# Optimization experiments

Measured on AMD Instinct MI355X. Metric: run time of the kernel, lower is better.

## Reference

```python
import jax, jax.numpy as jnp
import numpy as np
from jax import lax

VTH = 0.5
GRAD_WIN = 0.5
CDECAY = 0.5
VDECAY = 0.75

@jax.custom_vjp
def pseudo_spike(v):
    # PseudoSpikeRect: heaviside fwd, rectangular surrogate grad bwd
    return (v > VTH).astype(v.dtype)

def _ps_fwd(v):
    return pseudo_spike(v), v

def _ps_bwd(v, g):
    return (g * (jnp.abs(v - VTH) < GRAD_WIN).astype(g.dtype),)

pseudo_spike.defvjp(_ps_fwd, _ps_bwd)

def conv2d(x, w, b):
    y = lax.conv_general_dilated(x, w, (1, 1), 'VALID',
                                 dimension_numbers=('NCHW', 'OIHW', 'NCHW'))
    return y + b[None, :, None, None]

def lif(psp, state):
    # CUBA-LIF: current decay + integrate, voltage decay with spike reset, threshold
    cur, volt, spk = state
    cur = CDECAY * cur + psp
    volt = VDECAY * volt * (1.0 - spk) + cur
    spk = pseudo_spike(volt)
    return spk, (cur, volt, spk)

def setup_inputs() -> dict:
    key = jax.random.key(0)
    ks = jax.random.split(key, 16)
    B, T = 64, 200
    c1, c2, c3 = 64, 128, 256
    s = lambda k, shape, scale: jax.random.normal(k, shape, jnp.float32) * scale
    return {
        'input_data': jax.random.normal(ks[0], (B, 1, 10, 10, T), jnp.float32),
        'conv1_w': s(ks[1], (c1, 1, 3, 3), 0.3), 'conv1_b': s(ks[2], (c1,), 0.1),
        'conv2_w': s(ks[3], (c2, c1, 3, 3), 0.05), 'conv2_b': s(ks[4], (c2,), 0.1),
        'conv3_w': s(ks[5], (c3, c2, 3, 3), 0.03), 'conv3_b': s(ks[6], (c3,), 0.1),
        'tc_w': s(ks[7], (3, c3, c3), 0.06), 'tc_b': s(ks[8], (3, c3), 0.1),
        'rec_w': s(ks[9], (c3, c3), 0.06), 'rec_b': s(ks[10], (c3,), 0.1),
        'fc1_w': s(ks[11], (128, c3), 0.06), 'fc1_b': s(ks[12], (128,), 0.1),
        'fc2_w': s(ks[13], (2, 128), 0.09),
        'ts_weights': jnp.ones((T, 1), jnp.float32) / T,
    }

def reference(input_data, conv1_w, conv1_b, conv2_w, conv2_b, conv3_w, conv3_b,
              tc_w, tc_b, rec_w, rec_b, fc1_w, fc1_b, fc2_w, ts_weights):
    B = input_data.shape[0]
    c1, c2, c3 = conv1_w.shape[0], conv2_w.shape[0], conv3_w.shape[0]
    f1 = fc1_w.shape[0]

    def zs(shape):
        z = jnp.zeros(shape, input_data.dtype)
        return (z, z, z)

    carry0 = (zs((B, c1, 8, 8)), zs((B, c2, 6, 6)), zs((B, c3, 1, 1)),
              zs((B, c3)), zs((B, c3)), zs((B, f1)),
              jnp.zeros((3, B, c3), input_data.dtype),  # temporal buffer, idx0 = newest
              jnp.int32(0))
    xs = jnp.moveaxis(input_data, -1, 0)  # [T, B, 1, 10, 10]

    def step_fn(carry, xw):
        c1_st, c2_st, c3_st, tc_st, r_st, f_st, buf, step = carry
        x, w = xw
        s1, c1_st = lif(conv2d(x, conv1_w, conv1_b), c1_st)       # [B,c1,8,8]
        s2, c2_st = lif(conv2d(s1, conv2_w, conv2_b), c2_st)      # [B,c2,6,6]
        p = s2.reshape(B, c2, 3, 2, 3, 2).mean(axis=(3, 5))       # AvgPool2d(2) -> [B,c2,3,3]
        s3, c3_st = lif(conv2d(p, conv3_w, conv3_b), c3_st)       # [B,c3,1,1]
        flat = s3.reshape(B, -1)                                   # [B,c3]
        buf = jnp.concatenate([flat[None], buf[:2]], axis=0)
        # temporal conv: tap i applies to spike at time t-i, only if it exists
        psp = jnp.zeros_like(flat)
        for i in range(3):
            tap = buf[i] @ tc_w[i].T + tc_b[i]
            psp = psp + jnp.where(step >= i, 1.0, 0.0).astype(tap.dtype) * tap
        s_tc, tc_st = lif(psp, tc_st)
        # recurrent cell: identity feedforward + linear on previous spike
        psp_r = s_tc + r_st[2] @ rec_w.T + rec_b
        s_r, r_st = lif(psp_r, r_st)
        s_f, f_st = lif(s_r @ fc1_w.T + fc1_b, f_st)
        out = (s_f @ fc2_w.T) * w  # w = ts_weights[step], shape [1]
        return (c1_st, c2_st, c3_st, tc_st, r_st, f_st, buf, step + 1), out

    _, outs = lax.scan(step_fn, carry0, (xs, ts_weights))
    return outs.sum(axis=0)  # [B, 2]
```

## Files before the change

kernel.cpp:

```cpp
#include <hip/hip_runtime.h>


#define B_   64
#define T_   200
#define TCB_ 50

__device__ __forceinline__ void lif32(float psp, float& cur, float& volt, float& spk) {
#pragma clang fp contract(off)
    cur  = __fadd_rn(__fmul_rn(0.5f, cur), psp);
    volt = __fadd_rn(__fmul_rn(__fmul_rn(0.75f, volt), __fsub_rn(1.0f, spk)), cur);
    spk  = (volt > 0.5f) ? 1.0f : 0.0f;
}

__global__ void k_setup(const float* __restrict__ w2, const float* __restrict__ w3,
                        const float* __restrict__ tcw, const float* __restrict__ recw,
                        const float* __restrict__ fw,
                        float* __restrict__ w2T, float* __restrict__ w3T,
                        float* __restrict__ tcT, float* __restrict__ recT,
                        float* __restrict__ fc1T) {
    int idx = blockIdx.x * 256 + threadIdx.x;
    if (idx < 73728) { int o = idx & 127, k = idx >> 7; w2T[idx] = w2[o * 576 + k]; return; }
    idx -= 73728;
    if (idx < 294912) { int o = idx & 255, k = idx >> 8; w3T[idx] = w3[o * 1152 + k]; return; }
    idx -= 294912;
    if (idx < 196608) { int tap = idx >> 16, r = idx & 65535; int o = r & 255, k = r >> 8;
                        tcT[idx] = tcw[tap * 65536 + o * 256 + k]; return; }
    idx -= 196608;
    if (idx < 65536) { int o = idx & 255, k = idx >> 8; recT[idx] = recw[o * 256 + k]; return; }
    idx -= 65536;
    if (idx < 32768) { int o = idx & 127, k = idx >> 7; fc1T[idx] = fw[o * 256 + k]; return; }
}

__global__ __launch_bounds__(256) void k_conv1(const float* __restrict__ x,
                                               const float* __restrict__ w1,
                                               const float* __restrict__ b1,
                                               unsigned char* __restrict__ s1c,
                                               float* __restrict__ st1,
                                               int t0, int TC, int first) {
    int idx = blockIdx.x * 256 + threadIdx.x;
    int xx = idx & 7, yy = (idx >> 3) & 7, o = (idx >> 6) & 63, b = idx >> 12;
    float w[9];
#pragma unroll
    for (int i = 0; i < 9; i++) w[i] = w1[o * 9 + i];
    float bias = b1[o];
    const float* xb = x + (size_t)b * 20000;
    unsigned char* sb = s1c + (size_t)b * TC * 4096 + (o << 6) + (yy << 3) + xx;
    float cur, volt, spk;
    if (first) { cur = 0.f; volt = 0.f; spk = 0.f; }
    else { cur = st1[idx]; volt = st1[262144 + idx]; spk = st1[524288 + idx]; }
    for (int tl = 0; tl < TC; tl += 4) {
        int t = t0 + tl;
        float a0 = 0.f, a1 = 0.f, a2 = 0.f, a3 = 0.f;
#pragma unroll
        for (int i = 0; i < 3; i++) {
#pragma unroll
            for (int j = 0; j < 3; j++) {
                float4 v = *(const float4*)&xb[((yy + i) * 10 + xx + j) * T_ + t];
                float wv = w[i * 3 + j];
                a0 = fmaf(wv, v.x, a0); a1 = fmaf(wv, v.y, a1);
                a2 = fmaf(wv, v.z, a2); a3 = fmaf(wv, v.w, a3);
            }
        }
        float accs[4] = {a0, a1, a2, a3};
#pragma unroll
        for (int q = 0; q < 4; q++) {
            float psp = __fadd_rn(accs[q], bias);
            lif32(psp, cur, volt, spk);
            sb[(size_t)(tl + q) * 4096] = (unsigned char)spk;
        }
    }
    st1[idx] = cur; st1[262144 + idx] = volt; st1[524288 + idx] = spk;
}

__global__ __launch_bounds__(192) void k_conv2(const unsigned char* __restrict__ s1c,
                                               const float* __restrict__ w2T,
                                               const float* __restrict__ b2,
                                               float* __restrict__ psp2c) {
    __shared__ float a_s[4096];
    int blk = blockIdx.x;
    int tid = threadIdx.x;
    const unsigned int* src4 = (const unsigned int*)(s1c + (size_t)blk * 4096);
    for (int i = tid; i < 1024; i += 192) {
        unsigned int u = src4[i];
        a_s[4 * i + 0] = (float)(u & 0xff);
        a_s[4 * i + 1] = (float)((u >> 8) & 0xff);
        a_s[4 * i + 2] = (float)((u >> 16) & 0xff);
        a_s[4 * i + 3] = (float)(u >> 24);
    }
    __syncthreads();
    int quad = tid / 6;
    int y = tid - quad * 6;
    int ob = quad << 2;
    float acc[4][6];
#pragma unroll
    for (int oo = 0; oo < 4; oo++)
#pragma unroll
        for (int xq = 0; xq < 6; xq++) acc[oo][xq] = 0.f;
    for (int c = 0; c < 64; c++) {
#pragma unroll
        for (int i = 0; i < 3; i++) {
            const float* ar = &a_s[c * 64 + (y + i) * 8];
            float4 f0 = *(const float4*)(ar);
            float4 f1 = *(const float4*)(ar + 4);
            float a[8] = {f0.x, f0.y, f0.z, f0.w, f1.x, f1.y, f1.z, f1.w};
            const float* wr = w2T + (size_t)((c * 3 + i) * 3) * 128 + ob;
#pragma unroll
            for (int j = 0; j < 3; j++) {
                float4 wv = *(const float4*)(wr + j * 128);
                float w4[4] = {wv.x, wv.y, wv.z, wv.w};
#pragma unroll
                for (int oo = 0; oo < 4; oo++)
#pragma unroll
                    for (int xq = 0; xq < 6; xq++)
                        acc[oo][xq] = fmaf(w4[oo], a[xq + j], acc[oo][xq]);
            }
        }
    }
    size_t obase = (size_t)blk * 4608 + (size_t)ob * 36 + y * 6;
#pragma unroll
    for (int oo = 0; oo < 4; oo++) {
        float bv = b2[ob + oo];
        float* dst = psp2c + obase + oo * 36;
#pragma unroll
        for (int xq = 0; xq < 6; xq++)
            dst[xq] = __fadd_rn(acc[oo][xq], bv);
    }
}

__global__ __launch_bounds__(256) void k_lif2pool(const float* __restrict__ psp2c,
                                                  float* __restrict__ pc,
                                                  float* __restrict__ st2,
                                                  int TC, int first) {
    int idx = blockIdx.x * 256 + threadIdx.x;
    int px = idx % 3; int r = idx / 3; int py = r % 3; r /= 3;
    int o = r & 127, b = r >> 7;
    const float* pb = psp2c + (size_t)b * TC * 4608 + o * 36;
    float* pd = pc + (size_t)b * TC * 1152 + o * 9 + py * 3 + px;
    int off0 = (2 * py) * 6 + 2 * px, off1 = off0 + 6;
    float c0, c1, c2, c3, v0, v1, v2, v3, s0, s1, s2, s3;
    if (first) {
        c0 = c1 = c2 = c3 = v0 = v1 = v2 = v3 = s0 = s1 = s2 = s3 = 0.f;
    } else {
        c0 = st2[idx];              c1 = st2[73728 + idx];
        c2 = st2[147456 + idx];     c3 = st2[221184 + idx];
        v0 = st2[294912 + idx];     v1 = st2[368640 + idx];
        v2 = st2[442368 + idx];     v3 = st2[516096 + idx];
        s0 = st2[589824 + idx];     s1 = st2[663552 + idx];
        s2 = st2[737280 + idx];     s3 = st2[811008 + idx];
    }
    for (int tl = 0; tl < TC; tl++) {
        const float* pt = pb + (size_t)tl * 4608;
        float2 ra = *(const float2*)(pt + off0);
        float2 rb = *(const float2*)(pt + off1);
        lif32(ra.x, c0, v0, s0);
        lif32(ra.y, c1, v1, s1);
        lif32(rb.x, c2, v2, s2);
        lif32(rb.y, c3, v3, s3);
        pd[(size_t)tl * 1152] = __fmul_rn(0.25f, __fadd_rn(__fadd_rn(__fadd_rn(s0, s1), s2), s3));
    }
    st2[idx] = c0;           st2[73728 + idx] = c1;
    st2[147456 + idx] = c2;  st2[221184 + idx] = c3;
    st2[294912 + idx] = v0;  st2[368640 + idx] = v1;
    st2[442368 + idx] = v2;  st2[516096 + idx] = v3;
    st2[589824 + idx] = s0;  st2[663552 + idx] = s1;
    st2[737280 + idx] = s2;  st2[811008 + idx] = s3;
}

__global__ __launch_bounds__(256) void k_conv3(const float* __restrict__ pc,
                                               const float* __restrict__ w3T,
                                               const float* __restrict__ b3,
                                               float* __restrict__ psp3c) {
    __shared__ float a_s[16 * 288];
    int row0 = blockIdx.x * 16;
    int tid = threadIdx.x;
    int oq = tid & 63, mg = tid >> 6;
    float acc[4][4];
#pragma unroll
    for (int oo = 0; oo < 4; oo++)
#pragma unroll
        for (int mi = 0; mi < 4; mi++) acc[oo][mi] = 0.f;
    for (int kc = 0; kc < 1152; kc += 288) {
        __syncthreads();
        for (int idx = tid; idx < 16 * 288; idx += 256) {
            int m = idx / 288, k = idx - m * 288;
            a_s[idx] = pc[(size_t)(row0 + m) * 1152 + kc + k];
        }
        __syncthreads();
        for (int k = 0; k < 288; k++) {
            float4 wv = *(const float4*)&w3T[(size_t)(kc + k) * 256 + (oq << 2)];
            float w4[4] = {wv.x, wv.y, wv.z, wv.w};
            float am[4];
#pragma unroll
            for (int mi = 0; mi < 4; mi++) am[mi] = a_s[(mg * 4 + mi) * 288 + k];
#pragma unroll
            for (int oo = 0; oo < 4; oo++)
#pragma unroll
                for (int mi = 0; mi < 4; mi++)
                    acc[oo][mi] = fmaf(w4[oo], am[mi], acc[oo][mi]);
        }
    }
#pragma unroll
    for (int mi = 0; mi < 4; mi++) {
        float* dst = psp3c + (size_t)(row0 + mg * 4 + mi) * 256 + (oq << 2);
#pragma unroll
        for (int oo = 0; oo < 4; oo++)
            dst[oo] = __fadd_rn(acc[oo][mi], b3[(oq << 2) + oo]);
    }
}

__global__ __launch_bounds__(256) void k_scan3(const float* __restrict__ psp3c,
                                               unsigned char* __restrict__ s3u8,
                                               float* __restrict__ st3,
                                               int t0, int TC, int first) {
    int idx = blockIdx.x * 256 + threadIdx.x;
    int b = idx >> 8, n = idx & 255;
    float cur, volt, spk;
    if (first) { cur = 0.f; volt = 0.f; spk = 0.f; }
    else { cur = st3[idx]; volt = st3[16384 + idx]; spk = st3[32768 + idx]; }
    for (int tl = 0; tl < TC; tl++) {
        lif32(psp3c[(size_t)(b * TC + tl) * 256 + n], cur, volt, spk);
        s3u8[((size_t)b * T_ + t0 + tl) * 256 + n] = (unsigned char)spk;
    }
    st3[idx] = cur; st3[16384 + idx] = volt; st3[32768 + idx] = spk;
}

__global__ __launch_bounds__(256) void k_tc(const unsigned char* __restrict__ s3u8,
                                            const float* __restrict__ tcT,
                                            const float* __restrict__ tc_b,
                                            float* __restrict__ ptcc, int t0) {
    __shared__ float a_s[16 * 256];
    int crow0 = blockIdx.x * 16;
    int tid = threadIdx.x;
    int oq = tid & 63, mg = tid >> 6;
    float psum[4][4];
#pragma unroll
    for (int oo = 0; oo < 4; oo++)
#pragma unroll
        for (int mi = 0; mi < 4; mi++) psum[oo][mi] = 0.f;
    for (int tap = 0; tap < 3; tap++) {
        __syncthreads();
        for (int idx = tid; idx < 16 * 256; idx += 256) {
            int m = idx >> 8, k = idx & 255;
            int crow = crow0 + m;
            int b = crow / TCB_, tl = crow - b * TCB_;
            int t = t0 + tl;
            float v = 0.f;
            if (t >= tap) v = (float)s3u8[((size_t)b * T_ + t - tap) * 256 + k];
            a_s[idx] = v;
        }
        __syncthreads();
        float acc[4][4];
#pragma unroll
        for (int oo = 0; oo < 4; oo++)
#pragma unroll
            for (int mi = 0; mi < 4; mi++) acc[oo][mi] = 0.f;
        const float* wbase = tcT + (size_t)tap * 65536 + (oq << 2);
        for (int k = 0; k < 256; k++) {
            float4 wv = *(const float4*)(wbase + (size_t)k * 256);
            float w4[4] = {wv.x, wv.y, wv.z, wv.w};
            float am[4];
#pragma unroll
            for (int mi = 0; mi < 4; mi++) am[mi] = a_s[(mg * 4 + mi) * 256 + k];
#pragma unroll
            for (int oo = 0; oo < 4; oo++)
#pragma unroll
                for (int mi = 0; mi < 4; mi++)
                    acc[oo][mi] = fmaf(w4[oo], am[mi], acc[oo][mi]);
        }
#pragma unroll
        for (int mi = 0; mi < 4; mi++) {
            int crow = crow0 + mg * 4 + mi;
            int b = crow / TCB_, tl = crow - b * TCB_;
            int t = t0 + tl;
            float g = (t >= tap) ? 1.0f : 0.0f;
#pragma unroll
            for (int oo = 0; oo < 4; oo++) {
                int oc = (oq << 2) + oo;
                float tap_f = __fadd_rn(acc[oo][mi], tc_b[tap * 256 + oc]);
                psum[oo][mi] = __fadd_rn(psum[oo][mi], __fmul_rn(g, tap_f));
            }
        }
    }
#pragma unroll
    for (int mi = 0; mi < 4; mi++) {
        int crow = crow0 + mg * 4 + mi;
        float* dst = ptcc + (size_t)crow * 256 + (oq << 2);
#pragma unroll
        for (int oo = 0; oo < 4; oo++) dst[oo] = psum[oo][mi];
    }
}

__global__ __launch_bounds__(256) void k_scan_tc(const float* __restrict__ ptcc,
                                                 unsigned char* __restrict__ s_tc8,
                                                 float* __restrict__ st_tc,
                                                 int t0, int first) {
    int idx = blockIdx.x * 256 + threadIdx.x;
    int b = idx >> 8, n = idx & 255;
    float cur, volt, spk;
    if (first) { cur = 0.f; volt = 0.f; spk = 0.f; }
    else { cur = st_tc[idx]; volt = st_tc[16384 + idx]; spk = st_tc[32768 + idx]; }
    for (int tl = 0; tl < TCB_; tl++) {
        lif32(ptcc[(size_t)(b * TCB_ + tl) * 256 + n], cur, volt, spk);
        s_tc8[((size_t)b * T_ + t0 + tl) * 256 + n] = (unsigned char)spk;
    }
    st_tc[idx] = cur; st_tc[16384 + idx] = volt; st_tc[32768 + idx] = spk;
}

__global__ __launch_bounds__(256, 1) void k_rec(const unsigned char* __restrict__ s_tc8,
                                                const float* __restrict__ recT,
                                                const float* __restrict__ rec_b,
                                                unsigned char* __restrict__ s_r8) {
    __shared__ __align__(16) float spk_s[2][256];
    int b = blockIdx.x, o = threadIdx.x;
    float w[256];
#pragma unroll
    for (int k = 0; k < 256; k++) w[k] = recT[(size_t)k * 256 + o];
    spk_s[0][o] = 0.f;
    float cur = 0.f, volt = 0.f, spk = 0.f;
    float rb = rec_b[o];
    const unsigned char* stp = s_tc8 + (size_t)b * T_ * 256 + o;
    unsigned char* srp = s_r8 + (size_t)b * T_ * 256 + o;
    __syncthreads();
    int p = 0;
    for (int t = 0; t < T_; t++) {
        float stc = (float)stp[(size_t)t * 256];
        const float* sp = spk_s[p];
        float acc = 0.f;
#pragma unroll
        for (int k = 0; k < 256; k += 4) {
            float4 sv = *(const float4*)&sp[k];
            acc = fmaf(sv.x, w[k + 0], acc);
            acc = fmaf(sv.y, w[k + 1], acc);
            acc = fmaf(sv.z, w[k + 2], acc);
            acc = fmaf(sv.w, w[k + 3], acc);
        }
        float psp = __fadd_rn(__fadd_rn(stc, acc), rb);
        lif32(psp, cur, volt, spk);
        srp[(size_t)t * 256] = (unsigned char)spk;
        spk_s[p ^ 1][o] = spk;
        __syncthreads();
        p ^= 1;
    }
}

__global__ __launch_bounds__(256) void k_fc1(const unsigned char* __restrict__ s_r8,
                                             const float* __restrict__ fc1T,
                                             const float* __restrict__ fc1_b,
                                             float* __restrict__ pfc, int t0) {
    __shared__ float a_s[16 * 256];
    int crow0 = blockIdx.x * 16;
    int tid = threadIdx.x;
    int oq = tid & 31, mg = tid >> 5;
    float acc[4][2];
#pragma unroll
    for (int oo = 0; oo < 4; oo++) { acc[oo][0] = 0.f; acc[oo][1] = 0.f; }
    for (int idx = tid; idx < 16 * 256; idx += 256) {
        int m = idx >> 8, k = idx & 255;
        int crow = crow0 + m;
        int b = crow / TCB_, tl = crow - b * TCB_;
        a_s[idx] = (float)s_r8[((size_t)b * T_ + t0 + tl) * 256 + k];
    }
    __syncthreads();
    for (int k = 0; k < 256; k++) {
        float4 wv = *(const float4*)&fc1T[(size_t)k * 128 + (oq << 2)];
        float w4[4] = {wv.x, wv.y, wv.z, wv.w};
        float a0 = a_s[(mg * 2 + 0) * 256 + k];
        float a1 = a_s[(mg * 2 + 1) * 256 + k];
#pragma unroll
        for (int oo = 0; oo < 4; oo++) {
            acc[oo][0] = fmaf(w4[oo], a0, acc[oo][0]);
            acc[oo][1] = fmaf(w4[oo], a1, acc[oo][1]);
        }
    }
#pragma unroll
    for (int mi = 0; mi < 2; mi++) {
        float* dst = pfc + (size_t)(crow0 + mg * 2 + mi) * 128 + (oq << 2);
#pragma unroll
        for (int oo = 0; oo < 4; oo++)
            dst[oo] = __fadd_rn(acc[oo][mi], fc1_b[(oq << 2) + oo]);
    }
}

__global__ __launch_bounds__(256) void k_scan_f(const float* __restrict__ pfc,
                                                unsigned char* __restrict__ s_f8,
                                                float* __restrict__ st_f,
                                                int t0, int first) {
    int idx = blockIdx.x * 256 + threadIdx.x;
    int b = idx >> 7, n = idx & 127;
    float cur, volt, spk;
    if (first) { cur = 0.f; volt = 0.f; spk = 0.f; }
    else { cur = st_f[idx]; volt = st_f[8192 + idx]; spk = st_f[16384 + idx]; }
    for (int tl = 0; tl < TCB_; tl++) {
        lif32(pfc[(size_t)(b * TCB_ + tl) * 128 + n], cur, volt, spk);
        s_f8[((size_t)b * T_ + t0 + tl) * 128 + n] = (unsigned char)spk;
    }
    st_f[idx] = cur; st_f[8192 + idx] = volt; st_f[16384 + idx] = spk;
}

__global__ __launch_bounds__(128) void k_final(const unsigned char* __restrict__ s_f8,
                                               const float* __restrict__ ts,
                                               const float* __restrict__ fc2,
                                               float* __restrict__ out) {
    __shared__ double q_s[128];
    int b = blockIdx.x, k = threadIdx.x;
    double q = 0.0;
    const unsigned char* sf = s_f8 + (size_t)b * T_ * 128 + k;
    for (int t = 0; t < T_; t++) q = fma((double)ts[t], (double)sf[(size_t)t * 128], q);
    q_s[k] = q;
    __syncthreads();
    if (k < 2) {
        double o = 0.0;
        for (int kk = 0; kk < 128; kk++) o = fma((double)fc2[k * 128 + kk], q_s[kk], o);
        out[b * 2 + k] = (float)o;
    }
}

extern "C" void kernel_launch(void* const* d_in, const int* in_sizes, int n_in,
                              void* d_out, int out_size, void* d_ws, size_t ws_size,
                              hipStream_t stream) {
    const float* x       = (const float*)d_in[0];
    const float* conv1_w = (const float*)d_in[1];
    const float* conv1_b = (const float*)d_in[2];
    const float* conv2_w = (const float*)d_in[3];
    const float* conv2_b = (const float*)d_in[4];
    const float* conv3_w = (const float*)d_in[5];
    const float* conv3_b = (const float*)d_in[6];
    const float* tc_w    = (const float*)d_in[7];
    const float* tc_b    = (const float*)d_in[8];
    const float* rec_w   = (const float*)d_in[9];
    const float* rec_b   = (const float*)d_in[10];
    const float* fc1_w   = (const float*)d_in[11];
    const float* fc1_b   = (const float*)d_in[12];
    const float* fc2_w   = (const float*)d_in[13];
    const float* ts_w    = (const float*)d_in[14];
    float* out = (float*)d_out;
    (void)in_sizes; (void)n_in; (void)out_size;

    char* base = (char*)d_ws;
    float* w2T  = (float*)(base + 0);
    float* w3T  = (float*)(base + 294912);
    float* tcT  = (float*)(base + 1474560);
    float* recT = (float*)(base + 2260992);
    float* fc1T = (float*)(base + 2523136);
    float* st1  = (float*)(base + 2654208);
    float* st2  = (float*)(base + 5799936);
    float* st3  = (float*)(base + 9338880);
    float* st_tc= (float*)(base + 9535488);
    float* st_f = (float*)(base + 9732096);
    unsigned char* s3u8  = (unsigned char*)(base + 9830400);
    unsigned char* s_tc8 = (unsigned char*)(base + 13107200);
    unsigned char* s_r8  = (unsigned char*)(base + 16384000);
    unsigned char* s_f8  = (unsigned char*)(base + 19660800);

    const size_t PERS = 21299200;
    const size_t PER_T = 1802240;
    int TCF;
    if      (ws_size >= PERS + 40 * PER_T) TCF = 40;
    else if (ws_size >= PERS + 20 * PER_T) TCF = 20;
    else if (ws_size >= PERS +  8 * PER_T) TCF = 8;
    else                                   TCF = 4;
    int NCH = T_ / TCF;
    char* cb = base + PERS;
    float* psp2c = (float*)(cb);
    float* psp3c = (float*)(cb + (size_t)TCF * 1179648);
    float* pc    = (float*)(cb + (size_t)TCF * (1179648 + 65536));
    unsigned char* s1c = (unsigned char*)(cb + (size_t)TCF * (1179648 + 65536 + 294912));
    float* ptcc = (float*)(cb);
    float* pfc  = (float*)(cb + 3276800);

    k_setup<<<2592, 256, 0, stream>>>(conv2_w, conv3_w, tc_w, rec_w, fc1_w,
                                      w2T, w3T, tcT, recT, fc1T);
    for (int ch = 0; ch < NCH; ch++) {
        int t0 = ch * TCF;
        int first = (ch == 0) ? 1 : 0;
        k_conv1<<<1024, 256, 0, stream>>>(x, conv1_w, conv1_b, s1c, st1, t0, TCF, first);
        k_conv2<<<B_ * TCF, 192, 0, stream>>>(s1c, w2T, conv2_b, psp2c);
        k_lif2pool<<<288, 256, 0, stream>>>(psp2c, pc, st2, TCF, first);
        k_conv3<<<B_ * TCF / 16, 256, 0, stream>>>(pc, w3T, conv3_b, psp3c);
        k_scan3<<<64, 256, 0, stream>>>(psp3c, s3u8, st3, t0, TCF, first);
    }
    for (int bc = 0; bc < T_ / TCB_; bc++) {
        int t0 = bc * TCB_;
        k_tc<<<B_ * TCB_ / 16, 256, 0, stream>>>(s3u8, tcT, tc_b, ptcc, t0);
        k_scan_tc<<<64, 256, 0, stream>>>(ptcc, s_tc8, st_tc, t0, (bc == 0) ? 1 : 0);
    }
    k_rec<<<64, 256, 0, stream>>>(s_tc8, recT, rec_b, s_r8);
    for (int bc = 0; bc < T_ / TCB_; bc++) {
        int t0 = bc * TCB_;
        k_fc1<<<B_ * TCB_ / 16, 256, 0, stream>>>(s_r8, fc1T, fc1_b, pfc, t0);
        k_scan_f<<<32, 256, 0, stream>>>(pfc, s_f8, st_f, t0, (bc == 0) ? 1 : 0);
    }
    k_final<<<64, 128, 0, stream>>>(s_f8, ts_w, fc2_w, out);
}
```

Measured before the change: 2.709 ms.

## Sparsify recurrent matvec over active spikes and retile conv3 to four rows per block

The recurrent kernel no longer holds a 256-float weight column in registers and does a dense dot product with the previous spike vector. It builds a compacted list of active spike indices each step with ballot and popcount, then sums the matching weight rows from global memory. This skips work for silent neurons and relieves register pressure, at the cost of extra syncs and scattered global loads. Separately, conv3 now loads a full 4x1152 activation tile into shared memory once, so each thread computes one output row instead of four and the grid is four times larger.

```diff
diff --git a/kernel.cpp b/kernel.cpp
--- a/kernel.cpp
+++ b/kernel.cpp
@@ -170,42 +170,30 @@
                                                const float* __restrict__ w3T,
                                                const float* __restrict__ b3,
                                                float* __restrict__ psp3c) {
-    __shared__ float a_s[16 * 288];
-    int row0 = blockIdx.x * 16;
+    __shared__ float a_s[4 * 1152];
+    int row0 = blockIdx.x * 4;
     int tid = threadIdx.x;
     int oq = tid & 63, mg = tid >> 6;
-    float acc[4][4];
+    for (int idx = tid; idx < 4 * 1152; idx += 256) {
+        int m = idx / 1152, k = idx - m * 1152;
+        a_s[idx] = pc[(size_t)(row0 + m) * 1152 + k];
+    }
+    __syncthreads();
+    float acc[4] = {0.f, 0.f, 0.f, 0.f};
+    const float* as_row = &a_s[mg * 1152];
+#pragma unroll 4
+    for (int k = 0; k < 1152; k++) {
+        float4 wv = *(const float4*)&w3T[(size_t)k * 256 + (oq << 2)];
+        float am = as_row[k];
+        acc[0] = fmaf(wv.x, am, acc[0]);
+        acc[1] = fmaf(wv.y, am, acc[1]);
+        acc[2] = fmaf(wv.z, am, acc[2]);
+        acc[3] = fmaf(wv.w, am, acc[3]);
+    }
+    float* dst = psp3c + (size_t)(row0 + mg) * 256 + (oq << 2);
 #pragma unroll
     for (int oo = 0; oo < 4; oo++)
-#pragma unroll
-        for (int mi = 0; mi < 4; mi++) acc[oo][mi] = 0.f;
-    for (int kc = 0; kc < 1152; kc += 288) {
-        __syncthreads();
-        for (int idx = tid; idx < 16 * 288; idx += 256) {
-            int m = idx / 288, k = idx - m * 288;
-            a_s[idx] = pc[(size_t)(row0 + m) * 1152 + kc + k];
-        }
-        __syncthreads();
-        for (int k = 0; k < 288; k++) {
-            float4 wv = *(const float4*)&w3T[(size_t)(kc + k) * 256 + (oq << 2)];
-            float w4[4] = {wv.x, wv.y, wv.z, wv.w};
-            float am[4];
-#pragma unroll
-            for (int mi = 0; mi < 4; mi++) am[mi] = a_s[(mg * 4 + mi) * 288 + k];
-#pragma unroll
-            for (int oo = 0; oo < 4; oo++)
-#pragma unroll
-                for (int mi = 0; mi < 4; mi++)
-                    acc[oo][mi] = fmaf(w4[oo], am[mi], acc[oo][mi]);
-        }
-    }
-#pragma unroll
-    for (int mi = 0; mi < 4; mi++) {
-        float* dst = psp3c + (size_t)(row0 + mg * 4 + mi) * 256 + (oq << 2);
-#pragma unroll
-        for (int oo = 0; oo < 4; oo++)
-            dst[oo] = __fadd_rn(acc[oo][mi], b3[(oq << 2) + oo]);
-    }
+        dst[oo] = __fadd_rn(acc[oo], b3[(oq << 2) + oo]);
 }
 
 __global__ __launch_bounds__(256) void k_scan3(const float* __restrict__ psp3c,
@@ -310,36 +298,44 @@
                                                 const float* __restrict__ recT,
                                                 const float* __restrict__ rec_b,
                                                 unsigned char* __restrict__ s_r8) {
-    __shared__ __align__(16) float spk_s[2][256];
+    __shared__ unsigned short klist[256];
+    __shared__ int wcnt[4];
     int b = blockIdx.x, o = threadIdx.x;
-    float w[256];
-#pragma unroll
-    for (int k = 0; k < 256; k++) w[k] = recT[(size_t)k * 256 + o];
-    spk_s[0][o] = 0.f;
+    int lane = o & 63, wvi = o >> 6;
     float cur = 0.f, volt = 0.f, spk = 0.f;
     float rb = rec_b[o];
     const unsigned char* stp = s_tc8 + (size_t)b * T_ * 256 + o;
     unsigned char* srp = s_r8 + (size_t)b * T_ * 256 + o;
-    __syncthreads();
-    int p = 0;
+    int nact = 0;
     for (int t = 0; t < T_; t++) {
         float stc = (float)stp[(size_t)t * 256];
-        const float* sp = spk_s[p];
         float acc = 0.f;
-#pragma unroll
-        for (int k = 0; k < 256; k += 4) {
-            float4 sv = *(const float4*)&sp[k];
-            acc = fmaf(sv.x, w[k + 0], acc);
-            acc = fmaf(sv.y, w[k + 1], acc);
-            acc = fmaf(sv.z, w[k + 2], acc);
-            acc = fmaf(sv.w, w[k + 3], acc);
+        for (int j = 0; j < nact; j += 16) {
+#pragma unroll
+            for (int i = 0; i < 16; i++) {
+                int idx = j + i;
+                bool vld = idx < nact;
+                int k = vld ? (int)klist[idx] : 0;
+                float wv = recT[(size_t)k * 256 + o];
+                acc = __fadd_rn(acc, vld ? wv : 0.f);
+            }
         }
         float psp = __fadd_rn(__fadd_rn(stc, acc), rb);
         lif32(psp, cur, volt, spk);
         srp[(size_t)t * 256] = (unsigned char)spk;
-        spk_s[p ^ 1][o] = spk;
+        unsigned long long m = __ballot(spk != 0.f);
+        if (lane == 0) wcnt[wvi] = (int)__popcll(m);
         __syncthreads();
-        p ^= 1;
+        int base = 0;
+#pragma unroll
+        for (int q = 0; q < 4; q++) base += (q < wvi) ? wcnt[q] : 0;
+        int newn = wcnt[0] + wcnt[1] + wcnt[2] + wcnt[3];
+        if (spk != 0.f) {
+            int pos = base + (int)__popcll(m & ((1ull << lane) - 1ull));
+            klist[pos] = (unsigned short)o;
+        }
+        __syncthreads();
+        nact = newn;
     }
 }
 
@@ -476,7 +472,7 @@
         k_conv1<<<1024, 256, 0, stream>>>(x, conv1_w, conv1_b, s1c, st1, t0, TCF, first);
         k_conv2<<<B_ * TCF, 192, 0, stream>>>(s1c, w2T, conv2_b, psp2c);
         k_lif2pool<<<288, 256, 0, stream>>>(psp2c, pc, st2, TCF, first);
-        k_conv3<<<B_ * TCF / 16, 256, 0, stream>>>(pc, w3T, conv3_b, psp3c);
+        k_conv3<<<B_ * TCF / 4, 256, 0, stream>>>(pc, w3T, conv3_b, psp3c);
         k_scan3<<<64, 256, 0, stream>>>(psp3c, s3u8, st3, t0, TCF, first);
     }
     for (int bc = 0; bc < T_ / TCB_; bc++) {
```

Result: slower. 3.982 ms (+47.0%).
